# Performance work log

Hardware: AMD Instinct MI355X
Metric: run time of the kernel (lower is better)

## Reference

```python
import jax, jax.numpy as jnp
import numpy as np

FP8_MAX = 448.0  # float8_e4m3 max finite value


def setup_inputs() -> dict:
    key = jax.random.key(0)
    k1, k2, k3, k4, k5 = jax.random.split(key, 5)
    B, S, IN, OUT = 8, 2048, 2048, 2048
    x = jax.random.normal(k1, (B, S, IN), dtype=jnp.float32)
    weight = jax.random.normal(k2, (OUT, IN), dtype=jnp.float32) * 0.02
    bias = jax.random.normal(k3, (OUT,), dtype=jnp.float32)
    # per-tensor scales, kept positive and away from zero
    scale_in = jax.random.uniform(k4, (1,), dtype=jnp.float32) * 0.09 + 0.01
    scale_w = jax.random.uniform(k5, (1,), dtype=jnp.float32) * 0.09 + 0.01
    return {"x": x, "weight": weight, "bias": bias,
            "scale_in": scale_in, "scale_w": scale_w}


def _fp8_quantize(x, scale):
    # divide by scale, saturate to fp8 range, cast to fp8 e4m3
    q = jnp.clip(x / scale, -FP8_MAX, FP8_MAX)
    return q.astype(jnp.float8_e4m3fn)


def reference(x, weight, bias, scale_in, scale_w):
    # quantize input and weight to fp8 (per-tensor scales)
    xq = _fp8_quantize(x, scale_in)            # [B,S,IN] fp8
    wq = _fp8_quantize(weight, scale_w)        # [OUT,IN] fp8
    # scaled matmul: accumulate in fp32, dequant with scale_a*scale_b, emit fp16
    acc = jnp.einsum('bsk,nk->bsn', xq.astype(jnp.float32), wq.astype(jnp.float32))
    out = (acc * (scale_in[0] * scale_w[0])).astype(jnp.float16)
    out = out + bias.astype(jnp.float16)       # trailing bias add at fp16
    return out
```

## Files before the change

kernel.cpp:

```cpp
#include <hip/hip_runtime.h>
#include <hip/hip_fp16.h>
#include <stdint.h>

#define MDIM 16384
#define NDIM 2048
#define KDIM 2048

typedef __attribute__((ext_vector_type(4))) float f32x4;
typedef __attribute__((ext_vector_type(4))) int   i32x4;
typedef __attribute__((ext_vector_type(8))) int   i32x8;

__device__ __forceinline__ unsigned f32_to_e4m3(float x) {
    float q = fminf(448.f, fmaxf(-448.f, x));
    unsigned ub = __float_as_uint(q);
    unsigned sgn = (ub >> 24) & 0x80u;
    float aq = fabsf(q);
    int E = (int)((__float_as_uint(aq) >> 23) & 0xff) - 127;
    if (E < -6) E = -6;
    float rq = __uint_as_float((unsigned)(130 - E) << 23);
    int m = (int)rintf(aq * rq);
    if (m == 16) { m = 8; E += 1; }
    unsigned bits;
    if (m < 8) bits = sgn | (unsigned)m;
    else       bits = sgn | ((unsigned)(E + 7) << 3) | (unsigned)(m - 8);
    return bits;
}

__device__ __forceinline__ void quant_span(const float* __restrict__ x,
                                           uint8_t* __restrict__ q, float sc,
                                           unsigned i0, unsigned stride,
                                           unsigned n16) {
    for (unsigned i = i0; i < n16; i += stride) {
        const float4* xp = (const float4*)(x + (size_t)i * 16);
        uint32_t w[4];
#pragma unroll
        for (int j = 0; j < 4; ++j) {
            float4 v = xp[j];
            unsigned b0 = f32_to_e4m3(v.x / sc);
            unsigned b1 = f32_to_e4m3(v.y / sc);
            unsigned b2 = f32_to_e4m3(v.z / sc);
            unsigned b3 = f32_to_e4m3(v.w / sc);
            w[j] = b0 | (b1 << 8) | (b2 << 16) | (b3 << 24);
        }
        ((uint4*)q)[i] = make_uint4(w[0], w[1], w[2], w[3]);
    }
}

__global__ void quant_both_kernel(const float* __restrict__ x,
                                  uint8_t* __restrict__ xq,
                                  const float* __restrict__ w,
                                  uint8_t* __restrict__ wq,
                                  const float* __restrict__ s_in,
                                  const float* __restrict__ s_w) {
    if (blockIdx.x < 2048) {
        unsigned i0 = blockIdx.x * blockDim.x + threadIdx.x;
        quant_span(x, xq, s_in[0], i0, 2048 * 256,
                   (unsigned)((size_t)MDIM * KDIM / 16));
    } else {
        unsigned i0 = (blockIdx.x - 2048) * blockDim.x + threadIdx.x;
        quant_span(w, wq, s_w[0], i0, 256 * 256,
                   (unsigned)((size_t)NDIM * KDIM / 16));
    }
}

#define BM 256
#define BN 256
#define BKB 128
#define NKT (KDIM / BKB)

__device__ __forceinline__ void gload_lds16(const uint8_t* g, uint8_t* l) {
    __builtin_amdgcn_global_load_lds(
        (const __attribute__((address_space(1))) void*)g,
        (__attribute__((address_space(3))) void*)l, 16, 0, 0);
}

__device__ __forceinline__ void barrier_fenced() {
    asm volatile("" ::: "memory");
    __builtin_amdgcn_s_barrier();
    asm volatile("" ::: "memory");
}

__global__ __launch_bounds__(512) void gemm_fp8_kernel(
    const uint8_t* __restrict__ Aq, const uint8_t* __restrict__ Bq,
    const float* __restrict__ bias, const float* __restrict__ s_in,
    const float* __restrict__ s_w, float* __restrict__ out) {

    extern __shared__ uint8_t lds[];

    int nwg = gridDim.x;
    int cpx = nwg >> 3;
    int bid = blockIdx.x;
    int swz = (bid & 7) * cpx + (bid >> 3);
    int tm = swz >> 3;
    int tn = swz & 7;
    int row0 = tm * BM;
    int col0 = tn * BN;

    int tid  = threadIdx.x;
    int lane = tid & 63;
    int wid  = tid >> 6;
    int wr = wid >> 2, wc = wid & 3;
    int r15 = lane & 15;
    int g   = lane >> 4;

    int perm0 = ((2 * g + r15) & 7) << 4;
    int perm1 = ((2 * g + 1 + r15) & 7) << 4;

    int pj[2] = {tid, 512 + tid};
    int rj[2], cj[2];
#pragma unroll
    for (int j = 0; j < 2; ++j) {
        rj[j] = pj[j] >> 3;
        cj[j] = ((pj[j] & 7) - (rj[j] & 7)) & 7;
    }
    size_t asrcoff[2], bsrcoff[2];
    int    adst[2], bdst[2];
#pragma unroll
    for (int j = 0; j < 2; ++j) {
        int ar = (rj[j] & 63) + ((rj[j] >> 6) << 7);
        asrcoff[j] = (size_t)ar * KDIM + cj[j] * 16;
        bsrcoff[j] = (size_t)rj[j] * KDIM + cj[j] * 16;
        adst[j] = pj[j] * 16;
        bdst[j] = 32768 + pj[j] * 16;
    }

    const uint8_t* Asrc = Aq + (size_t)row0 * KDIM;
    const uint8_t* Bsrc = Bq + (size_t)col0 * KDIM;

#define STAGE_A(U, KT, DST)                                                   \
    {                                                                         \
        _Pragma("unroll")                                                     \
        for (int j_ = 0; j_ < 2; ++j_)                                        \
            gload_lds16(Asrc + asrcoff[j_] + (size_t)(U) * 64 * KDIM +        \
                            (size_t)(KT) * BKB,                               \
                        (DST) + adst[j_] + (U) * 16384);                      \
    }
#define STAGE_B(U, KT, DST)                                                   \
    {                                                                         \
        _Pragma("unroll")                                                     \
        for (int j_ = 0; j_ < 2; ++j_)                                        \
            gload_lds16(Bsrc + bsrcoff[j_] + (size_t)(U) * 128 * KDIM +       \
                            (size_t)(KT) * BKB,                               \
                        (DST) + bdst[j_] + (U) * 16384);                      \
    }

    f32x4 acc[8][4];
#pragma unroll
    for (int m = 0; m < 8; ++m)
#pragma unroll
        for (int n = 0; n < 4; ++n)
            acc[m][n] = (f32x4){0.f, 0.f, 0.f, 0.f};

    {
        uint8_t* b0 = &lds[0];
        STAGE_A(0, 0, b0); STAGE_B(1, 0, b0); STAGE_B(0, 0, b0); STAGE_A(1, 0, b0);
        asm volatile("s_waitcnt vmcnt(2)" ::: "memory");
        barrier_fenced();
    }

    int aRowBase = wr * 64;
    int bUnit = (wc >> 1) * 1024;
    int bRowBase = (wc & 1) * 64;

    i32x8 bf[4], af[4];

#define LOAD_BF_H(bo, H)                                                      \
    _Pragma("unroll")                                                         \
    for (int n_ = 2 * (H); n_ < 2 * (H) + 2; ++n_) {                          \
        int rB = bRowBase + n_ * 16 + r15;                                    \
        const uint8_t* rp = lds + (bo) + 32768 + (bUnit + rB * 8) * 16;       \
        i32x4 lo = *(const i32x4*)(rp + perm0);                               \
        i32x4 hi = *(const i32x4*)(rp + perm1);                               \
        _Pragma("unroll")                                                     \
        for (int q_ = 0; q_ < 4; ++q_) { bf[n_][q_] = lo[q_]; bf[n_][4 + q_] = hi[q_]; } \
    }

#define LOAD_AF(bo, MH)                                                       \
    _Pragma("unroll")                                                         \
    for (int m_ = 0; m_ < 4; ++m_) {                                          \
        int rA = aRowBase + m_ * 16 + r15;                                    \
        const uint8_t* rp = lds + (bo) + ((MH) * 1024 + rA * 8) * 16;         \
        i32x4 lo = *(const i32x4*)(rp + perm0);                               \
        i32x4 hi = *(const i32x4*)(rp + perm1);                               \
        _Pragma("unroll")                                                     \
        for (int q_ = 0; q_ < 4; ++q_) { af[m_][q_] = lo[q_]; af[m_][4 + q_] = hi[q_]; } \
    }

#define MFMA_Q(MH, NH)                                                        \
    __builtin_amdgcn_s_setprio(1);                                            \
    _Pragma("unroll")                                                         \
    for (int m_ = 0; m_ < 4; ++m_)                                            \
        _Pragma("unroll")                                                     \
        for (int n_ = 2 * (NH); n_ < 2 * (NH) + 2; ++n_)                      \
            acc[(MH) * 4 + m_][n_] =                                          \
                __builtin_amdgcn_mfma_scale_f32_16x16x128_f8f6f4(             \
                    af[m_], bf[n_], acc[(MH) * 4 + m_][n_],                   \
                    0, 0, 0, 127, 0, 127);                                    \
    __builtin_amdgcn_s_setprio(0);

    for (int t = 0; t < NKT; ++t) {
        const unsigned bo = (unsigned)(t & 1) << 16;
        uint8_t* obuf = &lds[(unsigned)((t + 1) & 1) << 16];
        LOAD_AF(bo, 0);
        LOAD_BF_H(bo, 0);
        if (t + 1 < NKT) { STAGE_A(0, t + 1, obuf); STAGE_B(1, t + 1, obuf); }
        MFMA_Q(0, 0);
        LOAD_BF_H(bo, 1);
        if (t + 1 < NKT) { STAGE_B(0, t + 1, obuf); }
        MFMA_Q(0, 1);
        if (t + 1 < NKT) asm volatile("s_waitcnt vmcnt(6)" ::: "memory");
        else             asm volatile("s_waitcnt vmcnt(0)" ::: "memory");
        barrier_fenced();
        LOAD_AF(bo, 1);
        MFMA_Q(1, 0);
        if (t + 1 < NKT) { STAGE_A(1, t + 1, obuf); }
        MFMA_Q(1, 1);
        if (t + 1 < NKT) asm volatile("s_waitcnt vmcnt(2)" ::: "memory");
        barrier_fenced();
    }

    float s = s_in[0] * s_w[0];
    float* slab = (float*)lds;
    __half hb[4];
#pragma unroll
    for (int n = 0; n < 4; ++n)
        hb[n] = __float2half(bias[col0 + wc * 64 + n * 16 + r15]);

#pragma unroll
    for (int mh = 0; mh < 2; ++mh) {
#pragma unroll
        for (int n = 0; n < 4; ++n) {
            int colb = wc * 64 + n * 16 + r15;
#pragma unroll
            for (int m = 0; m < 4; ++m) {
                int sr = wr * 64 + m * 16 + g * 4;
#pragma unroll
                for (int r = 0; r < 4; ++r) {
                    __half h = __float2half(acc[mh * 4 + m][n][r] * s);
                    slab[(sr + r) * 256 + colb] = __half2float(__hadd(h, hb[n]));
                }
            }
        }
        barrier_fenced();
#pragma unroll
        for (int it = 0; it < 16; ++it) {
            int srow = wid * 16 + it;
            f32x4 vv = *(const f32x4*)&slab[srow * 256 + lane * 4];
            int grow = row0 + (srow >> 6) * 128 + mh * 64 + (srow & 63);
            *(f32x4*)&out[(size_t)grow * NDIM + col0 + lane * 4] = vv;
        }
        barrier_fenced();
    }
#undef STAGE_A
#undef STAGE_B
#undef LOAD_BF_H
#undef LOAD_AF
#undef MFMA_Q
}

extern "C" void kernel_launch(void* const* d_in, const int* in_sizes, int n_in,
                              void* d_out, int out_size, void* d_ws, size_t ws_size,
                              hipStream_t stream) {
    const float* x      = (const float*)d_in[0];
    const float* weight = (const float*)d_in[1];
    const float* bias   = (const float*)d_in[2];
    const float* s_in   = (const float*)d_in[3];
    const float* s_w    = (const float*)d_in[4];
    float* out          = (float*)d_out;

    uint8_t* xq = (uint8_t*)d_ws;
    uint8_t* wq = (uint8_t*)d_ws + (size_t)MDIM * KDIM;

    quant_both_kernel<<<2304, 256, 0, stream>>>(x, xq, weight, wq, s_in, s_w);

    dim3 grid((MDIM / BM) * (NDIM / BN));
    gemm_fp8_kernel<<<grid, 512, 131072, stream>>>(xq, wq, bias, s_in, s_w, out);
}
```

Baseline: 119.8 us.

## Restructure GEMM main loop into barrier-separated quarter stages with B prefetched two tiles ahead

The main loop is reorganized so each K tile runs in four quarters, each with its own LDS fragment load, one global-to-LDS staging unit, barrier plus lgkmcnt wait, and MFMA block. B halves are now prefetched two tiles ahead while A is prefetched one ahead. The LDS layout for A changes to plain contiguous row halves, which simplifies addressing. The goal is finer interleaving of memory and MFMA work, at the cost of many more workgroup barriers per iteration and a tighter double-buffer ordering that could stall waves or race.

```diff
diff --git a/kernel.cpp b/kernel.cpp
--- a/kernel.cpp
+++ b/kernel.cpp
@@ -36,11 +36,8 @@
 #pragma unroll
         for (int j = 0; j < 4; ++j) {
             float4 v = xp[j];
-            unsigned b0 = f32_to_e4m3(v.x / sc);
-            unsigned b1 = f32_to_e4m3(v.y / sc);
-            unsigned b2 = f32_to_e4m3(v.z / sc);
-            unsigned b3 = f32_to_e4m3(v.w / sc);
-            w[j] = b0 | (b1 << 8) | (b2 << 16) | (b3 << 24);
+            w[j] = f32_to_e4m3(v.x / sc) | (f32_to_e4m3(v.y / sc) << 8) |
+                   (f32_to_e4m3(v.z / sc) << 16) | (f32_to_e4m3(v.w / sc) << 24);
         }
         ((uint4*)q)[i] = make_uint4(w[0], w[1], w[2], w[3]);
     }
@@ -53,11 +50,11 @@
                                   const float* __restrict__ s_in,
                                   const float* __restrict__ s_w) {
     if (blockIdx.x < 2048) {
-        unsigned i0 = blockIdx.x * blockDim.x + threadIdx.x;
+        unsigned i0 = blockIdx.x * 256 + threadIdx.x;
         quant_span(x, xq, s_in[0], i0, 2048 * 256,
                    (unsigned)((size_t)MDIM * KDIM / 16));
     } else {
-        unsigned i0 = (blockIdx.x - 2048) * blockDim.x + threadIdx.x;
+        unsigned i0 = (blockIdx.x - 2048) * 256 + threadIdx.x;
         quant_span(w, wq, s_w[0], i0, 256 * 256,
                    (unsigned)((size_t)NDIM * KDIM / 16));
     }
@@ -74,7 +71,7 @@
         (__attribute__((address_space(3))) void*)l, 16, 0, 0);
 }
 
-__device__ __forceinline__ void barrier_fenced() {
+__device__ __forceinline__ void barrier_raw() {
     asm volatile("" ::: "memory");
     __builtin_amdgcn_s_barrier();
     asm volatile("" ::: "memory");
@@ -106,42 +103,24 @@
     int perm0 = ((2 * g + r15) & 7) << 4;
     int perm1 = ((2 * g + 1 + r15) & 7) << 4;
 
-    int pj[2] = {tid, 512 + tid};
-    int rj[2], cj[2];
-#pragma unroll
-    for (int j = 0; j < 2; ++j) {
-        rj[j] = pj[j] >> 3;
-        cj[j] = ((pj[j] & 7) - (rj[j] & 7)) & 7;
-    }
-    size_t asrcoff[2], bsrcoff[2];
-    int    adst[2], bdst[2];
-#pragma unroll
-    for (int j = 0; j < 2; ++j) {
-        int ar = (rj[j] & 63) + ((rj[j] >> 6) << 7);
-        asrcoff[j] = (size_t)ar * KDIM + cj[j] * 16;
-        bsrcoff[j] = (size_t)rj[j] * KDIM + cj[j] * 16;
-        adst[j] = pj[j] * 16;
-        bdst[j] = 32768 + pj[j] * 16;
-    }
+    int up0 = tid, up1 = 512 + tid;
+    int ur0 = up0 >> 3, uc0 = ((up0 & 7) - (ur0 & 7)) & 7;
+    int ur1 = up1 >> 3, uc1 = ((up1 & 7) - (ur1 & 7)) & 7;
 
     const uint8_t* Asrc = Aq + (size_t)row0 * KDIM;
     const uint8_t* Bsrc = Bq + (size_t)col0 * KDIM;
 
-#define STAGE_A(U, KT, DST)                                                   \
+#define STAGE_U(MAT, H, KT)                                                   \
     {                                                                         \
-        _Pragma("unroll")                                                     \
-        for (int j_ = 0; j_ < 2; ++j_)                                        \
-            gload_lds16(Asrc + asrcoff[j_] + (size_t)(U) * 64 * KDIM +        \
-                            (size_t)(KT) * BKB,                               \
-                        (DST) + adst[j_] + (U) * 16384);                      \
-    }
-#define STAGE_B(U, KT, DST)                                                   \
-    {                                                                         \
-        _Pragma("unroll")                                                     \
-        for (int j_ = 0; j_ < 2; ++j_)                                        \
-            gload_lds16(Bsrc + bsrcoff[j_] + (size_t)(U) * 128 * KDIM +       \
-                            (size_t)(KT) * BKB,                               \
-                        (DST) + bdst[j_] + (U) * 16384);                      \
+        uint8_t* dst_ = &lds[(((unsigned)(KT) & 1) << 16) + (MAT) * 32768 +   \
+                             (H) * 16384];                                    \
+        const uint8_t* src_ = (MAT) ? Bsrc : Asrc;                            \
+        gload_lds16(src_ + (size_t)((H) * 128 + ur0) * KDIM +                 \
+                        (size_t)(KT) * BKB + uc0 * 16,                        \
+                    dst_ + up0 * 16);                                         \
+        gload_lds16(src_ + (size_t)((H) * 128 + ur1) * KDIM +                 \
+                        (size_t)(KT) * BKB + uc1 * 16,                        \
+                    dst_ + up1 * 16);                                         \
     }
 
     f32x4 acc[8][4];
@@ -151,42 +130,32 @@
         for (int n = 0; n < 4; ++n)
             acc[m][n] = (f32x4){0.f, 0.f, 0.f, 0.f};
 
-    {
-        uint8_t* b0 = &lds[0];
-        STAGE_A(0, 0, b0); STAGE_B(1, 0, b0); STAGE_B(0, 0, b0); STAGE_A(1, 0, b0);
-        asm volatile("s_waitcnt vmcnt(2)" ::: "memory");
-        barrier_fenced();
-    }
-
-    int aRowBase = wr * 64;
-    int bUnit = (wc >> 1) * 1024;
-    int bRowBase = (wc & 1) * 64;
-
-    i32x8 bf[4], af[4];
-
-#define LOAD_BF_H(bo, H)                                                      \
+    i32x8 af[4], bf[4];
+
+    int aRow0 = wr * 128 + r15;
+    int bRow0 = (wc >> 1) * 128 + (wc & 1) * 64 + r15;
+
+#define LOAD_AF(bo, MH)                                                       \
     _Pragma("unroll")                                                         \
-    for (int n_ = 2 * (H); n_ < 2 * (H) + 2; ++n_) {                          \
-        int rB = bRowBase + n_ * 16 + r15;                                    \
-        const uint8_t* rp = lds + (bo) + 32768 + (bUnit + rB * 8) * 16;       \
+    for (int m_ = 0; m_ < 4; ++m_) {                                          \
+        const uint8_t* rp = lds + (bo) + (aRow0 + (MH) * 64 + m_ * 16) * 128; \
+        i32x4 lo = *(const i32x4*)(rp + perm0);                               \
+        i32x4 hi = *(const i32x4*)(rp + perm1);                               \
+        _Pragma("unroll")                                                     \
+        for (int q_ = 0; q_ < 4; ++q_) { af[m_][q_] = lo[q_]; af[m_][4 + q_] = hi[q_]; } \
+    }
+
+#define LOAD_BF2(bo, NH)                                                      \
+    _Pragma("unroll")                                                         \
+    for (int n_ = 2 * (NH); n_ < 2 * (NH) + 2; ++n_) {                        \
+        const uint8_t* rp = lds + (bo) + 32768 + (bRow0 + n_ * 16) * 128;     \
         i32x4 lo = *(const i32x4*)(rp + perm0);                               \
         i32x4 hi = *(const i32x4*)(rp + perm1);                               \
         _Pragma("unroll")                                                     \
         for (int q_ = 0; q_ < 4; ++q_) { bf[n_][q_] = lo[q_]; bf[n_][4 + q_] = hi[q_]; } \
     }
 
-#define LOAD_AF(bo, MH)                                                       \
-    _Pragma("unroll")                                                         \
-    for (int m_ = 0; m_ < 4; ++m_) {                                          \
-        int rA = aRowBase + m_ * 16 + r15;                                    \
-        const uint8_t* rp = lds + (bo) + ((MH) * 1024 + rA * 8) * 16;         \
-        i32x4 lo = *(const i32x4*)(rp + perm0);                               \
-        i32x4 hi = *(const i32x4*)(rp + perm1);                               \
-        _Pragma("unroll")                                                     \
-        for (int q_ = 0; q_ < 4; ++q_) { af[m_][q_] = lo[q_]; af[m_][4 + q_] = hi[q_]; } \
-    }
-
-#define MFMA_Q(MH, NH)                                                        \
+#define MFMA8(MH, NH)                                                         \
     __builtin_amdgcn_s_setprio(1);                                            \
     _Pragma("unroll")                                                         \
     for (int m_ = 0; m_ < 4; ++m_)                                            \
@@ -198,25 +167,37 @@
                     0, 0, 0, 127, 0, 127);                                    \
     __builtin_amdgcn_s_setprio(0);
 
+#define LGKM0 asm volatile("s_waitcnt lgkmcnt(0)" ::: "memory")
+
+    STAGE_U(0, 0, 0); STAGE_U(0, 1, 0); STAGE_U(1, 0, 0); STAGE_U(1, 1, 0);
+    STAGE_U(1, 0, 1); STAGE_U(1, 1, 1);
+    asm volatile("s_waitcnt vmcnt(4)" ::: "memory");
+    barrier_raw();
+
     for (int t = 0; t < NKT; ++t) {
         const unsigned bo = (unsigned)(t & 1) << 16;
-        uint8_t* obuf = &lds[(unsigned)((t + 1) & 1) << 16];
         LOAD_AF(bo, 0);
-        LOAD_BF_H(bo, 0);
-        if (t + 1 < NKT) { STAGE_A(0, t + 1, obuf); STAGE_B(1, t + 1, obuf); }
-        MFMA_Q(0, 0);
-        LOAD_BF_H(bo, 1);
-        if (t + 1 < NKT) { STAGE_B(0, t + 1, obuf); }
-        MFMA_Q(0, 1);
-        if (t + 1 < NKT) asm volatile("s_waitcnt vmcnt(6)" ::: "memory");
+        LOAD_BF2(bo, 0);
+        if (t + 1 < NKT) STAGE_U(0, 0, t + 1);
+        barrier_raw(); LGKM0;
+        MFMA8(0, 0);
+        barrier_raw();
+        LOAD_BF2(bo, 1);
+        if (t + 1 < NKT) STAGE_U(0, 1, t + 1);
+        barrier_raw(); LGKM0;
+        MFMA8(0, 1);
+        barrier_raw();
+        LOAD_AF(bo, 1);
+        if (t + 2 < NKT) STAGE_U(1, 0, t + 2);
+        barrier_raw(); LGKM0;
+        MFMA8(1, 0);
+        barrier_raw();
+        if (t + 2 < NKT) STAGE_U(1, 1, t + 2);
+        barrier_raw(); LGKM0;
+        MFMA8(1, 1);
+        if (t + 2 < NKT) asm volatile("s_waitcnt vmcnt(4)" ::: "memory");
         else             asm volatile("s_waitcnt vmcnt(0)" ::: "memory");
-        barrier_fenced();
-        LOAD_AF(bo, 1);
-        MFMA_Q(1, 0);
-        if (t + 1 < NKT) { STAGE_A(1, t + 1, obuf); }
-        MFMA_Q(1, 1);
-        if (t + 1 < NKT) asm volatile("s_waitcnt vmcnt(2)" ::: "memory");
-        barrier_fenced();
+        barrier_raw();
     }
 
     float s = s_in[0] * s_w[0];
@@ -241,7 +222,7 @@
                 }
             }
         }
-        barrier_fenced();
+        barrier_raw();
 #pragma unroll
         for (int it = 0; it < 16; ++it) {
             int srow = wid * 16 + it;
@@ -249,13 +230,13 @@
             int grow = row0 + (srow >> 6) * 128 + mh * 64 + (srow & 63);
             *(f32x4*)&out[(size_t)grow * NDIM + col0 + lane * 4] = vv;
         }
-        barrier_fenced();
-    }
-#undef STAGE_A
-#undef STAGE_B
-#undef LOAD_BF_H
+        barrier_raw();
+    }
+#undef STAGE_U
 #undef LOAD_AF
-#undef MFMA_Q
+#undef LOAD_BF2
+#undef MFMA8
+#undef LGKM0
 }
 
 extern "C" void kernel_launch(void* const* d_in, const int* in_sizes, int n_in,
```

Measured after the change: 126.9 us. 5.9% more time.
